# Optimization experiments

Measured on AMD Instinct MI355X. Metric: run time of the kernel, lower is better.

The kernel has to match this reference:

```python
import jax, jax.numpy as jnp
import numpy as np

B, L, T, E, F, NB = 32, 512, 4096, 256, 256, 256


def _conv1d(x, w):
    # x: [B, T, Cin], w: [K, Cin, Cout], SAME padding (kernel 3, pad 1)
    return jax.lax.conv_general_dilated(x, w, (1,), 'SAME',
                                         dimension_numbers=('NWC', 'WIO', 'NWC'))


def _ln(h, scale, bias, eps=1e-5):
    m = h.mean(-1, keepdims=True)
    v = jnp.var(h, axis=-1, keepdims=True)
    return (h - m) * jax.lax.rsqrt(v + eps) * scale + bias


def _predict(x, mask, i, w1, b1, s1, bb1, w2, b2, s2, bb2, lw, lb):
    # FastSpeech2 VariancePredictor: conv-relu-ln (x2) -> linear to scalar, mask fill 0
    h = jax.nn.relu(_conv1d(x, w1[i]) + b1[i])
    h = _ln(h, s1[i], bb1[i])
    h = jax.nn.relu(_conv1d(h, w2[i]) + b2[i])
    h = _ln(h, s2[i], bb2[i])
    out = jnp.einsum('btf,f->bt', h, lw[i]) + lb[i]
    return jnp.where(mask, 0.0, out)


def _length_regulate(x, dur, t_max):
    # Expand x[b, l] dur[b, l] times along time, pad with zeros to t_max.
    cs = jnp.cumsum(dur, axis=1)                         # [B, L]
    t = jnp.arange(t_max)                                # [T]
    idx = jax.vmap(lambda c: jnp.searchsorted(c, t, side='right'))(cs)  # [B, T]
    valid = t[None, :] < cs[:, -1:]                      # [B, T]
    idx = jnp.minimum(idx, x.shape[1] - 1)
    xe = jnp.take_along_axis(x, idx[:, :, None], axis=1)  # [B, T, E]
    return jnp.where(valid[:, :, None], xe, 0.0)


def _bucket(v, bins):
    # torch.bucketize (right=False) == searchsorted side='left'; clip for embedding range
    return jnp.clip(jnp.searchsorted(bins, v, side='left'), 0, bins.shape[0] - 1)


def setup_inputs():
    key = jax.random.key(0)
    ks = jax.random.split(key, 12)
    def n(k, shape, s=0.02):
        return jax.random.normal(k, shape, dtype=jnp.float32) * s
    return dict(
        hidden_phoneme_sequence=jax.random.normal(ks[0], (B, L, E), dtype=jnp.float32),
        mask=jnp.zeros((B, L), dtype=bool),
        frame_mask=jnp.zeros((B, T), dtype=bool),
        duration_target=jax.random.randint(ks[1], (B, L), 0, 8, dtype=jnp.int32),
        pitch_target=jax.random.normal(ks[2], (B, T), dtype=jnp.float32),
        energy_target=jax.random.normal(ks[3], (B, T), dtype=jnp.float32),
        duration_scale=1,
        # stacked predictor params: index 0=duration, 1=pitch, 2=energy
        pred_w1=n(ks[4], (3, 3, E, F)),
        pred_b1=jnp.zeros((3, F), jnp.float32),
        ln1_s=jnp.ones((3, F), jnp.float32),
        ln1_b=jnp.zeros((3, F), jnp.float32),
        pred_w2=n(ks[5], (3, 3, F, F)),
        pred_b2=jnp.zeros((3, F), jnp.float32),
        ln2_s=jnp.ones((3, F), jnp.float32),
        ln2_b=jnp.zeros((3, F), jnp.float32),
        lin_w=n(ks[6], (3, F)),
        lin_b=jnp.zeros((3,), jnp.float32),
        pitch_bins=jnp.linspace(-3.0, 3.0, NB, dtype=jnp.float32),
        pitch_emb=n(ks[7], (NB, E), 1.0),
        energy_bins=jnp.linspace(-3.0, 3.0, NB, dtype=jnp.float32),
        energy_emb=n(ks[8], (NB, E), 1.0),
    )


def reference(hidden_phoneme_sequence, mask, frame_mask, duration_target,
              pitch_target, energy_target, duration_scale,
              pred_w1, pred_b1, ln1_s, ln1_b, pred_w2, pred_b2, ln2_s, ln2_b,
              lin_w, lin_b, pitch_bins, pitch_emb, energy_bins, energy_emb):
    P = (pred_w1, pred_b1, ln1_s, ln1_b, pred_w2, pred_b2, ln2_s, ln2_b, lin_w, lin_b)
    log_d = _predict(hidden_phoneme_sequence, mask, 0, *P)
    rounded_duration = jnp.maximum(jnp.round(jnp.exp(log_d) * duration_scale), 0.0)
    # training branch: expand with target durations
    x = _length_regulate(hidden_phoneme_sequence, duration_target, T)
    pitch = _predict(x, frame_mask, 1, *P)
    x = x + pitch_emb[_bucket(pitch_target, pitch_bins)]
    energy = _predict(x, frame_mask, 2, *P)
    variance_embedding = x + energy_emb[_bucket(energy_target, energy_bins)]
    return rounded_duration, pitch, energy, variance_embedding
```

## Files before the change

### kernel.cpp

```cpp
#include <hip/hip_runtime.h>
#include <stdint.h>

typedef unsigned short u16;
typedef unsigned int u32;

#define B_ 32
#define L_ 512
#define T_ 4096
#define E_ 256
#define F_ 256

#define TW 16
#define NH (TW + 2)
#define NX (TW + 4)
#define RS 20

#define MTW 62
#define MROWS 64
#define XROWS 66
#define XSTR 264
#define NBLK 67
#define KW 768
#define WMAT (KW * F_)

typedef short bf16x8 __attribute__((ext_vector_type(8)));
typedef float f32x4 __attribute__((ext_vector_type(4)));
union Frag { uint4 u; bf16x8 b; };

__device__ __forceinline__ u16 f2b(float f) {
    union { u32 i; float f; } x; x.f = f;
    u32 r = x.i + 0x7FFFu + ((x.i >> 16) & 1u);
    return (u16)(r >> 16);
}

__device__ __forceinline__ u32 cvt_pk(float lo, float hi) {
    u32 r;
    asm("v_cvt_pk_bf16_f32 %0, %1, %2" : "=v"(r) : "v"(lo), "v"(hi));
    return r;
}
__device__ __forceinline__ u16 f2b1(float f) {
    u32 r;
    asm("v_cvt_pk_bf16_f32 %0, %1, %2" : "=v"(r) : "v"(f), "v"(f));
    return (u16)r;
}

__global__ void prep_w_kernel(const float* __restrict__ W1all,
                              const float* __restrict__ W2all,
                              u16* __restrict__ dst) {
    const int g = blockIdx.x * 256 + threadIdx.x;
    const int mat = g / WMAT, rem = g % WMAT;
    const int kk = rem >> 8, f = rem & 255;
    const float* src = ((mat & 1) ? W2all : W1all) + ((mat >> 1) + 1) * (3 * E_ * F_);
    dst[mat * WMAT + f * KW + kk] = f2b(src[kk * 256 + f]);
}

__global__ __launch_bounds__(512) void cumsum_kernel(const int* __restrict__ dur,
                                                     int* __restrict__ csg) {
    __shared__ int cs[L_];
    const int b = blockIdx.x, tid = threadIdx.x;
    cs[tid] = dur[b * L_ + tid];
    __syncthreads();
    for (int off = 1; off < L_; off <<= 1) {
        int t = (tid >= off) ? cs[tid - off] : 0;
        __syncthreads();
        cs[tid] += t;
        __syncthreads();
    }
    csg[b * L_ + tid] = cs[tid];
}

__device__ __forceinline__ void conv_gemm(const u16* xs, const u16* __restrict__ WT,
                                          int col0, int nl, int quad, f32x4 acc[4][4]) {
#pragma unroll
    for (int mt = 0; mt < 4; ++mt)
#pragma unroll
        for (int nt = 0; nt < 4; ++nt) acc[mt][nt] = (f32x4){0.f, 0.f, 0.f, 0.f};
    const u16* wp0 = WT + (size_t)col0 * KW + quad * 8;
    Frag bq[4], bn[4];
#pragma unroll
    for (int nt = 0; nt < 4; ++nt) bq[nt].u = *(const uint4*)(wp0 + nt * (16 * KW));
    for (int s = 0; s < 24; ++s) {
        const int sp = (s + 1 < 24) ? s + 1 : 0;
#pragma unroll
        for (int nt = 0; nt < 4; ++nt)
            bn[nt].u = *(const uint4*)(wp0 + nt * (16 * KW) + sp * 32);
        const int kh = s >> 3, c0 = (s & 7) * 32;
        Frag a[4];
#pragma unroll
        for (int mt = 0; mt < 4; ++mt)
            a[mt].u = *(const uint4*)&xs[(16 * mt + nl + kh) * XSTR + c0 + quad * 8];
        __builtin_amdgcn_s_setprio(1);
#pragma unroll
        for (int mt = 0; mt < 4; ++mt)
#pragma unroll
            for (int nt = 0; nt < 4; ++nt)
                acc[mt][nt] = __builtin_amdgcn_mfma_f32_16x16x32_bf16(
                    a[mt].b, bq[nt].b, acc[mt][nt], 0, 0, 0);
        __builtin_amdgcn_s_setprio(0);
#pragma unroll
        for (int nt = 0; nt < 4; ++nt) bq[nt] = bn[nt];
    }
}

__global__ __launch_bounds__(256) void mfma_pe_kernel(
    const float* __restrict__ hidden, const int* __restrict__ csg,
    const float* __restrict__ pt, const float* __restrict__ pbins,
    const float* __restrict__ pemb,
    const float* __restrict__ et, const float* __restrict__ ebins,
    const float* __restrict__ eemb, float* __restrict__ ve,
    const u16* __restrict__ wt,
    const float* __restrict__ b1a, const float* __restrict__ s1a, const float* __restrict__ bb1a,
    const float* __restrict__ b2a, const float* __restrict__ s2a, const float* __restrict__ bb2a,
    const float* __restrict__ lwa, const float* __restrict__ lba,
    float* __restrict__ out_pitch, float* __restrict__ out_energy) {
    __shared__ u16 xs[XROWS * XSTR];
    __shared__ float2 red[MROWS][4];
    __shared__ float m_l[MROWS], inv_l[MROWS];
    __shared__ int cs_l[L_];
    __shared__ float bins_l[256];
    __shared__ float bins2_l[256];
    __shared__ int idx_l[XROWS];
    __shared__ int kb_l[XROWS];
    __shared__ int kb2_l[XROWS];

    const int tid = threadIdx.x;
    const int lane = tid & 63, w = tid >> 6;
    const int nl = lane & 15, quad = lane >> 4;
    const int mat = blockIdx.x / (B_ * NBLK);
    const int rem = blockIdx.x % (B_ * NBLK);
    const int b = rem / NBLK, blk = rem % NBLK;
    const int t0 = blk * MTW;
    const float* Xb = hidden + (size_t)b * (L_ * E_);

    const u16* WT1 = wt + (size_t)(2 * mat) * WMAT;
    const u16* WT2 = wt + (size_t)(2 * mat + 1) * WMAT;
    const float* B1 = b1a + (1 + mat) * F_;
    const float* S1 = s1a + (1 + mat) * F_;
    const float* Bb1 = bb1a + (1 + mat) * F_;
    const float* B2 = b2a + (1 + mat) * F_;
    const float* S2 = s2a + (1 + mat) * F_;
    const float* Bb2 = bb2a + (1 + mat) * F_;
    const float* LW = lwa + (1 + mat) * F_;
    const float lbv = lba[1 + mat];
    float* outp = mat ? out_energy : out_pitch;

    cs_l[tid] = csg[b * L_ + tid];
    cs_l[tid + 256] = csg[b * L_ + 256 + tid];
    if (mat) { bins_l[tid] = pbins[tid]; bins2_l[tid] = ebins[tid]; }
    __syncthreads();
    if (tid < XROWS) {
        const int tt = t0 - 2 + tid;
        int lo = 0, hi = L_;
        while (lo < hi) { int mid = (lo + hi) >> 1; if (cs_l[mid] <= tt) lo = mid + 1; else hi = mid; }
        const bool val = (tt >= 0) && (tt < T_) && (tt < cs_l[L_ - 1]);
        idx_l[tid] = val ? (lo < L_ - 1 ? lo : L_ - 1) : -1;
        int kb = 0, kb2 = 0;
        if (mat && tt >= 0 && tt < T_) {
            const float v = pt[b * T_ + tt];
            int lo2 = 0, hi2 = 256;
            while (lo2 < hi2) { int mid = (lo2 + hi2) >> 1; if (bins_l[mid] < v) lo2 = mid + 1; else hi2 = mid; }
            kb = lo2 > 255 ? 255 : lo2;
            const float v2 = et[b * T_ + tt];
            int lo3 = 0, hi3 = 256;
            while (lo3 < hi3) { int mid = (lo3 + hi3) >> 1; if (bins2_l[mid] < v2) lo3 = mid + 1; else hi3 = mid; }
            kb2 = lo3 > 255 ? 255 : lo3;
        }
        kb_l[tid] = kb;
        kb2_l[tid] = kb2;
    }
    __syncthreads();

    for (int it = 0; it < 17; ++it) {
        const int e = it * 256 + tid;
        if (e < XROWS * 64) {
            const int row = e >> 6, c4 = e & 63;
            const int tt = t0 - 2 + row;
            float4 v = make_float4(0.f, 0.f, 0.f, 0.f);
            const int id = idx_l[row];
            if (id >= 0) v = *(const float4*)(Xb + (size_t)id * E_ + c4 * 4);
            if (mat && tt >= 0 && tt < T_) {
                const float4 ev = *(const float4*)(pemb + (size_t)kb_l[row] * E_ + c4 * 4);
                v.x += ev.x; v.y += ev.y; v.z += ev.z; v.w += ev.w;
                if (row >= 2 && row < 64) {
                    const float4 ee = *(const float4*)(eemb + (size_t)kb2_l[row] * E_ + c4 * 4);
                    float4 o = make_float4(v.x + ee.x, v.y + ee.y, v.z + ee.z, v.w + ee.w);
                    *(float4*)(ve + ((size_t)(b * T_ + tt)) * E_ + c4 * 4) = o;
                }
            }
            uint2 pk = make_uint2(cvt_pk(v.x, v.y), cvt_pk(v.z, v.w));
            *(uint2*)&xs[row * XSTR + c4 * 4] = pk;
        }
    }
    __syncthreads();

    const int col0 = w * 64 + nl;
    f32x4 acc[4][4];

    conv_gemm(xs, WT1, col0, nl, quad, acc);

    float pb[4], ps[4], pbb[4];
#pragma unroll
    for (int nt = 0; nt < 4; ++nt) {
        pb[nt] = B1[col0 + nt * 16]; ps[nt] = S1[col0 + nt * 16]; pbb[nt] = Bb1[col0 + nt * 16];
    }
#pragma unroll
    for (int mt = 0; mt < 4; ++mt)
#pragma unroll
        for (int nt = 0; nt < 4; ++nt)
#pragma unroll
            for (int r = 0; r < 4; ++r)
                acc[mt][nt][r] = fmaxf(acc[mt][nt][r] + pb[nt], 0.f);
#pragma unroll
    for (int mt = 0; mt < 4; ++mt)
#pragma unroll
        for (int r = 0; r < 4; ++r) {
            float s = acc[mt][0][r] + acc[mt][1][r] + acc[mt][2][r] + acc[mt][3][r];
            float q = acc[mt][0][r] * acc[mt][0][r] + acc[mt][1][r] * acc[mt][1][r] +
                      acc[mt][2][r] * acc[mt][2][r] + acc[mt][3][r] * acc[mt][3][r];
#pragma unroll
            for (int off = 1; off < 16; off <<= 1) { s += __shfl_xor(s, off); q += __shfl_xor(q, off); }
            if (nl == 0) red[16 * mt + 4 * quad + r][w] = make_float2(s, q);
        }
    __syncthreads();
    if (tid < MROWS) {
        const float2 p0 = red[tid][0], p1 = red[tid][1], p2 = red[tid][2], p3 = red[tid][3];
        const float s = p0.x + p1.x + p2.x + p3.x, q = p0.y + p1.y + p2.y + p3.y;
        const float m = s * (1.f / 256.f);
        const float var = q * (1.f / 256.f) - m * m;
        m_l[tid] = m; inv_l[tid] = 1.f / sqrtf(var + 1e-5f);
    }
    __syncthreads();
#pragma unroll
    for (int mt = 0; mt < 4; ++mt)
#pragma unroll
        for (int r = 0; r < 4; ++r) {
            const int row = 16 * mt + 4 * quad + r;
            const int th = t0 - 1 + row;
            const float mm = m_l[row], iv = inv_l[row];
#pragma unroll
            for (int nt = 0; nt < 4; ++nt) {
                float y = (acc[mt][nt][r] - mm) * iv * ps[nt] + pbb[nt];
                if (th < 0 || th >= T_) y = 0.f;
                xs[row * XSTR + col0 + nt * 16] = f2b1(y);
            }
        }
    __syncthreads();

    conv_gemm(xs, WT2, col0, nl, quad, acc);

#pragma unroll
    for (int nt = 0; nt < 4; ++nt) {
        pb[nt] = B2[col0 + nt * 16]; ps[nt] = S2[col0 + nt * 16]; pbb[nt] = Bb2[col0 + nt * 16];
    }
#pragma unroll
    for (int mt = 0; mt < 4; ++mt)
#pragma unroll
        for (int nt = 0; nt < 4; ++nt)
#pragma unroll
            for (int r = 0; r < 4; ++r)
                acc[mt][nt][r] = fmaxf(acc[mt][nt][r] + pb[nt], 0.f);
#pragma unroll
    for (int mt = 0; mt < 4; ++mt)
#pragma unroll
        for (int r = 0; r < 4; ++r) {
            float s = acc[mt][0][r] + acc[mt][1][r] + acc[mt][2][r] + acc[mt][3][r];
            float q = acc[mt][0][r] * acc[mt][0][r] + acc[mt][1][r] * acc[mt][1][r] +
                      acc[mt][2][r] * acc[mt][2][r] + acc[mt][3][r] * acc[mt][3][r];
#pragma unroll
            for (int off = 1; off < 16; off <<= 1) { s += __shfl_xor(s, off); q += __shfl_xor(q, off); }
            if (nl == 0) red[16 * mt + 4 * quad + r][w] = make_float2(s, q);
        }
    __syncthreads();
    if (tid < MROWS) {
        const float2 p0 = red[tid][0], p1 = red[tid][1], p2 = red[tid][2], p3 = red[tid][3];
        const float s = p0.x + p1.x + p2.x + p3.x, q = p0.y + p1.y + p2.y + p3.y;
        const float m = s * (1.f / 256.f);
        const float var = q * (1.f / 256.f) - m * m;
        m_l[tid] = m; inv_l[tid] = 1.f / sqrtf(var + 1e-5f);
    }
    __syncthreads();
    float lwv[4];
#pragma unroll
    for (int nt = 0; nt < 4; ++nt) lwv[nt] = LW[col0 + nt * 16];
#pragma unroll
    for (int mt = 0; mt < 4; ++mt)
#pragma unroll
        for (int r = 0; r < 4; ++r) {
            const int row = 16 * mt + 4 * quad + r;
            const float mm = m_l[row], iv = inv_l[row];
            float z = 0.f;
#pragma unroll
            for (int nt = 0; nt < 4; ++nt) {
                const float y = (acc[mt][nt][r] - mm) * iv * ps[nt] + pbb[nt];
                z = fmaf(y, lwv[nt], z);
            }
#pragma unroll
            for (int off = 1; off < 16; off <<= 1) z += __shfl_xor(z, off);
            if (nl == 0) red[row][w].x = z;
        }
    __syncthreads();
    if (tid < MTW) {
        const int t = t0 + tid;
        if (t < T_) {
            const float z = red[tid][0].x + red[tid][1].x + red[tid][2].x + red[tid][3].x + lbv;
            outp[b * T_ + t] = z;
        }
    }
}

template <int MODE>
__global__ __launch_bounds__(256) void predictor_kernel(
    const float* __restrict__ X, const float* __restrict__ W1,
    const float* __restrict__ B1, const float* __restrict__ S1,
    const float* __restrict__ Bb1, const float* __restrict__ W2,
    const float* __restrict__ B2, const float* __restrict__ S2,
    const float* __restrict__ Bb2, const float* __restrict__ LW,
    const float* __restrict__ LB, const int* __restrict__ dscale,
    float* __restrict__ out, int S) {
    __shared__ float buf[E_ * RS];
    __shared__ float red_s[NH][4], red_q[NH][4];
    __shared__ float m_l[NH], inv_l[NH];

    const int tid = threadIdx.x;
    const int lane = tid & 63, wv = tid >> 6;
    const int m0 = blockIdx.x * TW;
    const int b = m0 / S;
    const int t0 = m0 % S;
    const float* Xb = X + (size_t)b * S * E_;

#pragma unroll
    for (int s = 0; s < NX; ++s) {
        const int tt = t0 - 2 + s;
        float v = 0.f;
        if (tt >= 0 && tt < S) v = Xb[(size_t)tt * E_ + tid];
        buf[tid * RS + s] = v;
    }
    __syncthreads();

    float a1[NH];
#pragma unroll
    for (int r = 0; r < NH; ++r) a1[r] = 0.f;
    {
        const float* Wf = W1 + tid;
        for (int c = 0; c < E_; c += 4) {
            float wl[12];
#pragma unroll
            for (int cc = 0; cc < 4; ++cc) {
                wl[cc * 3 + 0] = Wf[(0 * E_ + c + cc) * F_];
                wl[cc * 3 + 1] = Wf[(1 * E_ + c + cc) * F_];
                wl[cc * 3 + 2] = Wf[(2 * E_ + c + cc) * F_];
            }
#pragma unroll
            for (int cc = 0; cc < 4; ++cc) {
                const float4* xq = (const float4*)(&buf[(c + cc) * RS]);
                const float4 q0 = xq[0], q1 = xq[1], q2 = xq[2], q3 = xq[3], q4 = xq[4];
                const float xr[NX] = {q0.x, q0.y, q0.z, q0.w, q1.x, q1.y, q1.z, q1.w,
                                      q2.x, q2.y, q2.z, q2.w, q3.x, q3.y, q3.z, q3.w,
                                      q4.x, q4.y, q4.z, q4.w};
                const float w0 = wl[cc * 3 + 0], w1 = wl[cc * 3 + 1], w2 = wl[cc * 3 + 2];
#pragma unroll
                for (int r = 0; r < NH; ++r) {
                    a1[r] = fmaf(xr[r],     w0, a1[r]);
                    a1[r] = fmaf(xr[r + 1], w1, a1[r]);
                    a1[r] = fmaf(xr[r + 2], w2, a1[r]);
                }
            }
        }
    }
    __syncthreads();

    const float b1f = B1[tid];
#pragma unroll
    for (int r = 0; r < NH; ++r) a1[r] = fmaxf(a1[r] + b1f, 0.f);

#pragma unroll
    for (int r = 0; r < NH; ++r) {
        float s = a1[r], q = a1[r] * a1[r];
#pragma unroll
        for (int off = 32; off; off >>= 1) { s += __shfl_xor(s, off); q += __shfl_xor(q, off); }
        if (lane == 0) { red_s[r][wv] = s; red_q[r][wv] = q; }
    }
    __syncthreads();
    if (tid < NH) {
        const float s = red_s[tid][0] + red_s[tid][1] + red_s[tid][2] + red_s[tid][3];
        const float q = red_q[tid][0] + red_q[tid][1] + red_q[tid][2] + red_q[tid][3];
        const float m = s * (1.f / F_);
        const float v = q * (1.f / F_) - m * m;
        m_l[tid] = m;
        inv_l[tid] = 1.f / sqrtf(v + 1e-5f);
    }
    __syncthreads();

    const float s1f = S1[tid], sb1 = Bb1[tid];
#pragma unroll
    for (int r = 0; r < NH; ++r) {
        const int th = t0 - 1 + r;
        float y = (a1[r] - m_l[r]) * inv_l[r] * s1f + sb1;
        if (th < 0 || th >= S) y = 0.f;
        buf[tid * RS + r] = y;
    }
    __syncthreads();

    float a2[TW];
#pragma unroll
    for (int p = 0; p < TW; ++p) a2[p] = 0.f;
    {
        const float* Wf = W2 + tid;
        for (int c = 0; c < E_; c += 4) {
            float wl[12];
#pragma unroll
            for (int cc = 0; cc < 4; ++cc) {
                wl[cc * 3 + 0] = Wf[(0 * E_ + c + cc) * F_];
                wl[cc * 3 + 1] = Wf[(1 * E_ + c + cc) * F_];
                wl[cc * 3 + 2] = Wf[(2 * E_ + c + cc) * F_];
            }
#pragma unroll
            for (int cc = 0; cc < 4; ++cc) {
                const float4* xq = (const float4*)(&buf[(c + cc) * RS]);
                const float4 q0 = xq[0], q1 = xq[1], q2 = xq[2], q3 = xq[3], q4 = xq[4];
                const float xr[NX] = {q0.x, q0.y, q0.z, q0.w, q1.x, q1.y, q1.z, q1.w,
                                      q2.x, q2.y, q2.z, q2.w, q3.x, q3.y, q3.z, q3.w,
                                      q4.x, q4.y, q4.z, q4.w};
                const float w0 = wl[cc * 3 + 0], w1 = wl[cc * 3 + 1], w2 = wl[cc * 3 + 2];
#pragma unroll
                for (int p = 0; p < TW; ++p) {
                    a2[p] = fmaf(xr[p],     w0, a2[p]);
                    a2[p] = fmaf(xr[p + 1], w1, a2[p]);
                    a2[p] = fmaf(xr[p + 2], w2, a2[p]);
                }
            }
        }
    }

    const float b2f = B2[tid];
    float r_[TW];
#pragma unroll
    for (int p = 0; p < TW; ++p) r_[p] = fmaxf(a2[p] + b2f, 0.f);

#pragma unroll
    for (int p = 0; p < TW; ++p) {
        float s = r_[p], q = r_[p] * r_[p];
#pragma unroll
        for (int off = 32; off; off >>= 1) { s += __shfl_xor(s, off); q += __shfl_xor(q, off); }
        if (lane == 0) { red_s[p][wv] = s; red_q[p][wv] = q; }
    }
    __syncthreads();
    if (tid < TW) {
        const float s = red_s[tid][0] + red_s[tid][1] + red_s[tid][2] + red_s[tid][3];
        const float q = red_q[tid][0] + red_q[tid][1] + red_q[tid][2] + red_q[tid][3];
        const float m = s * (1.f / F_);
        const float v = q * (1.f / F_) - m * m;
        m_l[tid] = m;
        inv_l[tid] = 1.f / sqrtf(v + 1e-5f);
    }
    __syncthreads();

    const float s2f = S2[tid], sb2 = Bb2[tid];
    const float lwf = LW[tid];
#pragma unroll
    for (int p = 0; p < TW; ++p) {
        const float y = (r_[p] - m_l[p]) * inv_l[p] * s2f + sb2;
        float z = y * lwf;
#pragma unroll
        for (int off = 32; off; off >>= 1) z += __shfl_xor(z, off);
        if (lane == 0) red_s[p][wv] = z;
    }
    __syncthreads();
    if (tid < TW) {
        float z = red_s[tid][0] + red_s[tid][1] + red_s[tid][2] + red_s[tid][3] + LB[0];
        if (MODE == 1) {
            const float e = expf(z) * (float)dscale[0];
            z = fmaxf(rintf(e), 0.f);
        }
        out[m0 + tid] = z;
    }
}

extern "C" void kernel_launch(void* const* d_in, const int* in_sizes, int n_in,
                              void* d_out, int out_size, void* d_ws, size_t ws_size,
                              hipStream_t stream) {
    (void)in_sizes; (void)n_in; (void)ws_size; (void)out_size;
    const float* hidden = (const float*)d_in[0];
    const int*   dur    = (const int*)d_in[3];
    const float* pt     = (const float*)d_in[4];
    const float* et     = (const float*)d_in[5];
    const int*   dscale = (const int*)d_in[6];
    const float* w1  = (const float*)d_in[7];
    const float* b1  = (const float*)d_in[8];
    const float* s1  = (const float*)d_in[9];
    const float* bb1 = (const float*)d_in[10];
    const float* w2  = (const float*)d_in[11];
    const float* b2  = (const float*)d_in[12];
    const float* s2  = (const float*)d_in[13];
    const float* bb2 = (const float*)d_in[14];
    const float* lw  = (const float*)d_in[15];
    const float* lb  = (const float*)d_in[16];
    const float* pbins = (const float*)d_in[17];
    const float* pemb  = (const float*)d_in[18];
    const float* ebins = (const float*)d_in[19];
    const float* eemb  = (const float*)d_in[20];

    float* out        = (float*)d_out;
    float* out_dur    = out;
    float* out_pitch  = out + 16384;
    float* out_energy = out + 147456;
    float* ove        = out + 278528;

    u16* wt = (u16*)d_ws;
    int* csg = (int*)(wt + 4 * WMAT);

    prep_w_kernel<<<(4 * WMAT) / 256, 256, 0, stream>>>(w1, w2, wt);

    cumsum_kernel<<<B_, 512, 0, stream>>>(dur, csg);

    predictor_kernel<1><<<(B_ * L_) / TW, 256, 0, stream>>>(
        hidden, w1, b1, s1, bb1, w2, b2, s2, bb2, lw, lb, dscale, out_dur, L_);

    mfma_pe_kernel<<<2 * B_ * NBLK, 256, 0, stream>>>(
        hidden, csg, pt, pbins, pemb, et, ebins, eemb, ove, wt,
        b1, s1, bb1, b2, s2, bb2, lw, lb,
        out_pitch, out_energy);
}
```

Before: 854.8 us.

## Add occupancy hint to MFMA kernel and restructure duration predictor input loads

Adds a minimum-blocks-per-CU hint of 3 to the main MFMA pitch/energy kernel, so the compiler has to cap register use. In the scalar duration-predictor kernel, the shared-memory staging of the input window and its barrier are dropped, and each thread reads the 20 input values straight from global memory in the inner loop. The second conv loop is changed to load two channels' LDS rows at once before issuing the FMAs. The direct global reads are wave-uniform broadcasts but happen far more often than before. The launch-bounds hint may cause register spills.

New measurement: 1.088 ms. +27.3%, slower.

```diff
diff --git a/kernel.cpp b/kernel.cpp
--- a/kernel.cpp
+++ b/kernel.cpp
@@ -102,7 +102,7 @@
     }
 }
 
-__global__ __launch_bounds__(256) void mfma_pe_kernel(
+__global__ __launch_bounds__(256, 3) void mfma_pe_kernel(
     const float* __restrict__ hidden, const int* __restrict__ csg,
     const float* __restrict__ pt, const float* __restrict__ pbins,
     const float* __restrict__ pemb,
@@ -328,15 +328,6 @@
     const int t0 = m0 % S;
     const float* Xb = X + (size_t)b * S * E_;
 
-#pragma unroll
-    for (int s = 0; s < NX; ++s) {
-        const int tt = t0 - 2 + s;
-        float v = 0.f;
-        if (tt >= 0 && tt < S) v = Xb[(size_t)tt * E_ + tid];
-        buf[tid * RS + s] = v;
-    }
-    __syncthreads();
-
     float a1[NH];
 #pragma unroll
     for (int r = 0; r < NH; ++r) a1[r] = 0.f;
@@ -352,11 +343,12 @@
             }
 #pragma unroll
             for (int cc = 0; cc < 4; ++cc) {
-                const float4* xq = (const float4*)(&buf[(c + cc) * RS]);
-                const float4 q0 = xq[0], q1 = xq[1], q2 = xq[2], q3 = xq[3], q4 = xq[4];
-                const float xr[NX] = {q0.x, q0.y, q0.z, q0.w, q1.x, q1.y, q1.z, q1.w,
-                                      q2.x, q2.y, q2.z, q2.w, q3.x, q3.y, q3.z, q3.w,
-                                      q4.x, q4.y, q4.z, q4.w};
+                float xr[NX];
+#pragma unroll
+                for (int s = 0; s < NX; ++s) {
+                    const int tt = t0 - 2 + s;
+                    xr[s] = (tt >= 0 && tt < S) ? Xb[(size_t)tt * E_ + (c + cc)] : 0.f;
+                }
                 const float w0 = wl[cc * 3 + 0], w1 = wl[cc * 3 + 1], w2 = wl[cc * 3 + 2];
 #pragma unroll
                 for (int r = 0; r < NH; ++r) {
@@ -367,7 +359,6 @@
             }
         }
     }
-    __syncthreads();
 
     const float b1f = B1[tid];
 #pragma unroll
@@ -415,18 +406,34 @@
                 wl[cc * 3 + 2] = Wf[(2 * E_ + c + cc) * F_];
             }
 #pragma unroll
-            for (int cc = 0; cc < 4; ++cc) {
-                const float4* xq = (const float4*)(&buf[(c + cc) * RS]);
-                const float4 q0 = xq[0], q1 = xq[1], q2 = xq[2], q3 = xq[3], q4 = xq[4];
-                const float xr[NX] = {q0.x, q0.y, q0.z, q0.w, q1.x, q1.y, q1.z, q1.w,
-                                      q2.x, q2.y, q2.z, q2.w, q3.x, q3.y, q3.z, q3.w,
-                                      q4.x, q4.y, q4.z, q4.w};
-                const float w0 = wl[cc * 3 + 0], w1 = wl[cc * 3 + 1], w2 = wl[cc * 3 + 2];
-#pragma unroll
-                for (int p = 0; p < TW; ++p) {
-                    a2[p] = fmaf(xr[p],     w0, a2[p]);
-                    a2[p] = fmaf(xr[p + 1], w1, a2[p]);
-                    a2[p] = fmaf(xr[p + 2], w2, a2[p]);
+            for (int h = 0; h < 4; h += 2) {
+                const float4* xqa = (const float4*)(&buf[(c + h) * RS]);
+                const float4* xqb = (const float4*)(&buf[(c + h + 1) * RS]);
+                const float4 a0 = xqa[0], a1q = xqa[1], a2q = xqa[2], a3q = xqa[3], a4q = xqa[4];
+                const float4 b0 = xqb[0], b1q = xqb[1], b2q = xqb[2], b3q = xqb[3], b4q = xqb[4];
+                {
+                    const float xr[NX] = {a0.x, a0.y, a0.z, a0.w, a1q.x, a1q.y, a1q.z, a1q.w,
+                                          a2q.x, a2q.y, a2q.z, a2q.w, a3q.x, a3q.y, a3q.z, a3q.w,
+                                          a4q.x, a4q.y, a4q.z, a4q.w};
+                    const float w0 = wl[h * 3 + 0], w1 = wl[h * 3 + 1], w2 = wl[h * 3 + 2];
+#pragma unroll
+                    for (int p = 0; p < TW; ++p) {
+                        a2[p] = fmaf(xr[p],     w0, a2[p]);
+                        a2[p] = fmaf(xr[p + 1], w1, a2[p]);
+                        a2[p] = fmaf(xr[p + 2], w2, a2[p]);
+                    }
+                }
+                {
+                    const float xr[NX] = {b0.x, b0.y, b0.z, b0.w, b1q.x, b1q.y, b1q.z, b1q.w,
+                                          b2q.x, b2q.y, b2q.z, b2q.w, b3q.x, b3q.y, b3q.z, b3q.w,
+                                          b4q.x, b4q.y, b4q.z, b4q.w};
+                    const float w0 = wl[(h + 1) * 3 + 0], w1 = wl[(h + 1) * 3 + 1], w2 = wl[(h + 1) * 3 + 2];
+#pragma unroll
+                    for (int p = 0; p < TW; ++p) {
+                        a2[p] = fmaf(xr[p],     w0, a2[p]);
+                        a2[p] = fmaf(xr[p + 1], w1, a2[p]);
+                        a2[p] = fmaf(xr[p + 2], w2, a2[p]);
+                    }
                 }
             }
         }
```
